# Kernel optimization log

Hardware: AMD Instinct MI355X
Metric: run time of the kernel (lower is better)

Reference implementation:

```python
import jax, jax.numpy as jnp
import numpy as np

V = 30522   # bert-base-uncased vocab
E = 512     # embed_size
ATT = 512   # attention_dim
ENC = 2048  # encoder_dim
H = 512     # decoder_dim
B = 32
N = 49      # num image features (7x7)
T = 21      # caption length -> 20 decode steps


def setup_inputs() -> dict:
    key = jax.random.key(0)
    ks = jax.random.split(key, 12)
    s = lambda i, shape: jax.random.normal(ks[i], shape, jnp.float32) * 0.02
    features = jax.random.normal(ks[0], (B, N, ENC), jnp.float32)
    captions = jax.random.randint(ks[1], (B, T), 0, V, dtype=jnp.int32)
    return dict(
        features=features, captions=captions,
        emb=s(2, (V, E)),
        W_w=s(3, (ATT, H)), W_b=jnp.zeros((ATT,), jnp.float32),
        U_w=s(4, (ATT, ENC)), U_b=jnp.zeros((ATT,), jnp.float32),
        A_w=s(5, (1, ATT)), A_b=jnp.zeros((1,), jnp.float32),
        init_h_w=s(6, (H, ENC)), init_h_b=jnp.zeros((H,), jnp.float32),
        init_c_w=s(7, (H, ENC)), init_c_b=jnp.zeros((H,), jnp.float32),
        w_ih=s(8, (4 * H, E + ENC)), w_hh=s(9, (4 * H, H)),
        b_ih=jnp.zeros((4 * H,), jnp.float32), b_hh=jnp.zeros((4 * H,), jnp.float32),
        fcn_w=s(10, (V, H)), fcn_b=jnp.zeros((V,), jnp.float32),
    )


def reference(features, captions, emb, W_w, W_b, U_w, U_b, A_w, A_b,
              init_h_w, init_h_b, init_c_w, init_c_b,
              w_ih, w_hh, b_ih, b_hh, fcn_w, fcn_b):
    embeds = emb[captions]                      # [B, T, E]
    mean_f = features.mean(axis=1)              # [B, ENC]
    h0 = mean_f @ init_h_w.T + init_h_b         # [B, H]
    c0 = mean_f @ init_c_w.T + init_c_b
    # U(features) is h-independent: precompute once (same math as per-step in torch)
    u_hs = jnp.einsum('bne,ae->bna', features, U_w) + U_b  # [B, N, ATT]

    def step(carry, x_t):
        h, c = carry
        # Bahdanau attention
        w_ah = h @ W_w.T + W_b                               # [B, ATT]
        scores = jnp.tanh(u_hs + w_ah[:, None, :]) @ A_w[0] + A_b[0]  # [B, N]
        alpha = jax.nn.softmax(scores, axis=1)
        context = jnp.einsum('bn,bne->be', alpha, features)  # [B, ENC]
        # LSTMCell (torch gate order: i, f, g, o)
        lstm_in = jnp.concatenate([x_t, context], axis=1)    # [B, E+ENC]
        gates = lstm_in @ w_ih.T + b_ih + h @ w_hh.T + b_hh  # [B, 4H]
        i, f, g, o = jnp.split(gates, 4, axis=1)
        c2 = jax.nn.sigmoid(f) * c + jax.nn.sigmoid(i) * jnp.tanh(g)
        h2 = jax.nn.sigmoid(o) * jnp.tanh(c2)
        # dropout in eval mode = identity
        out = h2 @ fcn_w.T + fcn_b                           # [B, V]
        return (h2, c2), (out, alpha)

    xs = jnp.swapaxes(embeds[:, :-1], 0, 1)  # [T-1, B, E]
    _, (preds, alphas) = jax.lax.scan(step, (h0, c0), xs)
    return jnp.swapaxes(preds, 0, 1), jnp.swapaxes(alphas, 0, 1)
```

## Files before the change

### kernel.cpp

```cpp
#include <hip/hip_runtime.h>
#include <hip/hip_bf16.h>

#define VCB 30522
#define EMB 512
#define ATTD 512
#define ENC 2048
#define HD 512
#define BB 32
#define NF 49
#define TSTEPS 20
#define EIN 2560
#define KCAT 3072
#define WSTRIDE 3080
#define DTPB 512

typedef __attribute__((ext_vector_type(8))) __bf16 bf16x8;
typedef __attribute__((ext_vector_type(4))) __bf16 bf16x4;
typedef __attribute__((ext_vector_type(4))) float floatx4;
typedef __hip_bfloat16 bf16;

__device__ __forceinline__ float bf2f(bf16 x){ return __bfloat162float(x); }
__device__ __forceinline__ bf16 f2bf(float x){ return __float2bfloat16(x); }
__device__ __forceinline__ float sigm(float x){ return 1.0f/(1.0f+expf(-x)); }
__device__ __forceinline__ float fast_tanh(float x){
    float e2 = __expf(2.0f*x);
    return 1.0f - 2.0f*__builtin_amdgcn_rcpf(e2 + 1.0f);
}

__device__ __forceinline__ float ld1(const void* base, size_t idx, int f){
    if (f) return ((const float*)base)[idx];
    return bf2f(((const bf16*)base)[idx]);
}
__device__ __forceinline__ bf16x8 ldbf8(const void* base, size_t idx, int f){
    if (f){
        const float* p = (const float*)base + idx;
        float4 a = *(const float4*)p, b = *(const float4*)(p+4);
        bf16x8 r;
        r[0]=(__bf16)a.x; r[1]=(__bf16)a.y; r[2]=(__bf16)a.z; r[3]=(__bf16)a.w;
        r[4]=(__bf16)b.x; r[5]=(__bf16)b.y; r[6]=(__bf16)b.z; r[7]=(__bf16)b.w;
        return r;
    }
    return *(const bf16x8*)((const bf16*)base + idx);
}
__device__ __forceinline__ bf16x8 bf8_of_f32(const float* p){
    float4 a = *(const float4*)p, b = *(const float4*)(p+4);
    bf16x8 r;
    r[0]=(__bf16)a.x; r[1]=(__bf16)a.y; r[2]=(__bf16)a.z; r[3]=(__bf16)a.w;
    r[4]=(__bf16)b.x; r[5]=(__bf16)b.y; r[6]=(__bf16)b.z; r[7]=(__bf16)b.w;
    return r;
}
__device__ __forceinline__ void st1(void* base, size_t idx, float v, int f){
    if (f) ((float*)base)[idx] = v;
    else   ((bf16*)base)[idx] = f2bf(v);
}

#define MFMA16(a,b,c) __builtin_amdgcn_mfma_f32_16x16x32_bf16(a,b,c,0,0,0)

__device__ __forceinline__ void gbar(unsigned* bar, unsigned ep){
    __syncthreads();
    if (threadIdx.x == 0){
        unsigned tgt = ep*16u;
        unsigned* grp  = bar + ((blockIdx.x >> 4) << 4);
        unsigned* root = bar + 256;
        unsigned old = __hip_atomic_fetch_add(grp, 1u, __ATOMIC_ACQ_REL, __HIP_MEMORY_SCOPE_AGENT);
        if (old + 1u == tgt)
            __hip_atomic_fetch_add(root, 1u, __ATOMIC_ACQ_REL, __HIP_MEMORY_SCOPE_AGENT);
        while (__hip_atomic_load(root, __ATOMIC_RELAXED, __HIP_MEMORY_SCOPE_AGENT) < tgt)
            __builtin_amdgcn_s_sleep(2);
        __builtin_amdgcn_fence(__ATOMIC_ACQUIRE, "agent");
    }
    __syncthreads();
}

__global__ void k_detect(const void* emb, int* flag, unsigned* bar){
    int tid = threadIdx.x;
    __shared__ int bad;
    if (tid == 0) bad = 0;
    for (int i = tid; i < 512; i += 256) bar[i] = 0u;
    __syncthreads();
    const unsigned short* u = (const unsigned short*)emb;
    int local = 0;
    for (int i = tid; i < 4096; i += 256){
        int e = (u[i] >> 7) & 0xFF;
        if (e > 140) local = 1;
    }
    if (local) bad = 1;
    __syncthreads();
    if (tid == 0) *flag = bad;
}

__global__ void k_prep_gates(const void* w_ih, const void* w_hh, bf16* __restrict__ wcat,
                             const int* __restrict__ flag){
    int ff = *flag;
    int r = blockIdx.x, tid = threadIdx.x;
    for (int i = tid*8; i < KCAT; i += 2048){
        bf16x8 v;
        if (i + 8 <= EIN){
            v = ldbf8(w_ih, (size_t)r*EIN + i, ff);
        } else if (i >= EIN){
            v = ldbf8(w_hh, (size_t)r*HD + (i - EIN), ff);
        } else {
#pragma unroll
            for (int j = 0; j < 8; ++j){
                int k = i + j;
                v[j] = (__bf16)((k < EIN) ? ld1(w_ih, (size_t)r*EIN + k, ff)
                                          : ld1(w_hh, (size_t)r*HD + (k - EIN), ff));
            }
        }
        *(bf16x8*)(wcat + (size_t)r*KCAT + i) = v;
    }
}
__global__ void k_prep_cvt8(const void* src, bf16* __restrict__ dst, size_t n8,
                            const int* __restrict__ flag){
    int ff = *flag;
    size_t idx = (size_t)blockIdx.x*256 + threadIdx.x;
    size_t stride = (size_t)gridDim.x*256;
    for (size_t i = idx; i < n8; i += stride)
        *(bf16x8*)(dst + i*8) = ldbf8(src, i*8, ff);
}

__global__ void k_mean(const void* feat, float* __restrict__ mean_f,
                       const int* __restrict__ flag){
    int ff = *flag;
    int b = blockIdx.x, tid = threadIdx.x;
    for (int i = 0; i < ENC/256; ++i){
        int e = i*256 + tid;
        size_t base = (size_t)b*NF*ENC + e;
        float s = 0.f;
        for (int n = 0; n < NF; ++n) s += ld1(feat, base + (size_t)n*ENC, ff);
        mean_f[b*ENC + e] = s * (1.0f/49.0f);
    }
}

__global__ void k_init_hc(const float* __restrict__ mean_f,
                          const void* ihw, const void* ihb,
                          const void* icw, const void* icb,
                          float* __restrict__ Hbuf, float* __restrict__ c_f32,
                          const int* __restrict__ flag){
    int ff = *flag;
    int tid = threadIdx.x, wave = tid>>6, lane = tid&63, quad = lane>>4, lq = lane&15;
    int n0 = blockIdx.x*16;
    int ng = n0 + lq;
    const void* w = (ng < HD) ? ihw : icw;
    size_t wrow = (size_t)(ng < HD ? ng : ng - HD)*ENC;
    floatx4 acc[2] = {{0,0,0,0},{0,0,0,0}};
    int kb = wave*512;
    for (int kk = 0; kk < 16; ++kk){
        int k = kb + kk*32 + quad*8;
        bf16x8 bfr = ldbf8(w, wrow + k, ff);
#pragma unroll
        for (int mt = 0; mt < 2; ++mt){
            bf16x8 afr = bf8_of_f32(mean_f + (size_t)(mt*16+lq)*ENC + k);
            acc[mt] = MFMA16(afr, bfr, acc[mt]);
        }
    }
    __shared__ float red[4][2][16][16];
#pragma unroll
    for (int mt = 0; mt < 2; ++mt)
        for (int r = 0; r < 4; ++r)
            red[wave][mt][quad*4+r][lq] = acc[mt][r];
    __syncthreads();
    for (int rep = 0; rep < 2; ++rep){
        int idx = rep*256 + tid;
        int mt = idx>>8, mm = (idx>>4)&15, nn = idx&15;
        float v = red[0][mt][mm][nn]+red[1][mt][mm][nn]+red[2][mt][mm][nn]+red[3][mt][mm][nn];
        int n_g = n0 + nn, b = mt*16 + mm;
        if (n_g < HD) Hbuf[b*HD + n_g]        = v + ld1(ihb, n_g, ff);
        else          c_f32[b*HD + (n_g-HD)]  = v + ld1(icb, n_g - HD, ff);
    }
}

__global__ void k_uhs(const bf16* __restrict__ feat_bf, const void* U_w, const void* U_b,
                      float* __restrict__ u_hs, const int* __restrict__ flag){
    int ff = *flag;
    int tid = threadIdx.x, wave = tid>>6, lane = tid&63, quad = lane>>4, lq = lane&15;
    int m0 = blockIdx.x*16;
    int n0 = blockIdx.y*64 + wave*16;
    size_t arow = (size_t)(m0+lq)*ENC;
    size_t brow = (size_t)(n0+lq)*ENC;
    floatx4 acc = {0,0,0,0};
    for (int kk = 0; kk < ENC/32; ++kk){
        int k = kk*32 + quad*8;
        bf16x8 afr = *(const bf16x8*)(feat_bf + arow + k);
        bf16x8 bfr = ldbf8(U_w,  brow + k, ff);
        acc = MFMA16(afr, bfr, acc);
    }
    float ub = ld1(U_b, n0+lq, ff);
    for (int r = 0; r < 4; ++r){
        int m = m0 + quad*4 + r;
        u_hs[(size_t)m*ATTD + n0 + lq] = acc[r] + ub;
    }
}

__global__ void __launch_bounds__(DTPB) k_decode(
        float* __restrict__ Hbuf, const float* __restrict__ c0_f32,
        const bf16* __restrict__ Ww_bf, const void* __restrict__ W_b,
        const float* __restrict__ u_hs, const void* __restrict__ A_w,
        const void* __restrict__ A_b, const int* __restrict__ captions,
        const void* __restrict__ emb, const bf16* __restrict__ feat_bf,
        bf16* __restrict__ lstm_in, const bf16* __restrict__ wcat,
        const void* __restrict__ b_ih, const void* __restrict__ b_hh,
        bf16* __restrict__ Hall_bf, void* __restrict__ d_out,
        const int* __restrict__ flag, unsigned* __restrict__ bar)
{
    const int ff = *flag;
    const int bid = blockIdx.x, tid = threadIdx.x;
    const int wave = tid>>6, lane = tid&63, quad = lane>>4, lq = lane&15;

    __shared__ bf16  wlds[8*WSTRIDE];
    __shared__ float ubuf[2048];
    __shared__ float aw_s[ATTD];
    __shared__ float c_loc[64];
    __shared__ float gbias[8];

    for (int n = 0; n < 8; ++n){
        int g = n>>1, j = n&1;
        const bf16* src = wcat + (size_t)(g*HD + (bid<<1) + j)*KCAT;
        for (int c8 = tid; c8 < KCAT/8; c8 += DTPB)
            *(bf16x8*)(wlds + n*WSTRIDE + c8*8) = *(const bf16x8*)(src + c8*8);
    }
    if (tid < 64){
        int bb = tid&31, j = tid>>5, col = (bid<<1)+j;
        c_loc[bb*2+j] = c0_f32[bb*HD + col];
        lstm_in[(size_t)bb*KCAT + EIN + col] = f2bf(Hbuf[bb*HD + col]);
    }
    if (tid < 8){
        int g = tid>>1, j = tid&1, col = (bid<<1)+j;
        gbias[tid] = ld1(b_ih, g*HD+col, ff) + ld1(b_hh, g*HD+col, ff);
    }
    if (bid < BB)
        for (int i = tid; i < ATTD; i += DTPB) aw_s[i] = ld1(A_w, i, ff);
    __syncthreads();

    float* h_sh    = ubuf;
    float* wah_s   = ubuf + 512;
    float* sc_s    = ubuf + 1024;
    float* alpha_s = ubuf + 1088;
    float (*red)[2][16][16] = (float (*)[2][16][16])ubuf;

    unsigned ep = 0;

    for (int t = 0; t < TSTEPS; ++t){
        if (bid < BB){
            const int b = bid;
            const float* h_t = Hbuf + (size_t)t*BB*HD;
            for (int i = tid; i < HD; i += DTPB) h_sh[i] = h_t[b*HD + i];
            int cap = captions[b*21 + t];
            for (int e = tid; e < EMB; e += DTPB)
                lstm_in[(size_t)b*KCAT + e] = f2bf(ld1(emb, (size_t)cap*EMB + e, ff));
            __syncthreads();
            for (int a = tid; a < ATTD; a += DTPB){
                const bf16* wr = Ww_bf + (size_t)a*HD;
                float s0=0.f, s1=0.f, s2=0.f, s3=0.f;
                for (int k = 0; k < HD; k += 8){
                    bf16x8 wv = *(const bf16x8*)(wr + k);
                    s0 += (float)wv[0]*h_sh[k+0] + (float)wv[4]*h_sh[k+4];
                    s1 += (float)wv[1]*h_sh[k+1] + (float)wv[5]*h_sh[k+5];
                    s2 += (float)wv[2]*h_sh[k+2] + (float)wv[6]*h_sh[k+6];
                    s3 += (float)wv[3]*h_sh[k+3] + (float)wv[7]*h_sh[k+7];
                }
                wah_s[a] = ((s0+s1)+(s2+s3)) + ld1(W_b, a, ff);
            }
            __syncthreads();
            {
                int a0 = lane*8;
                for (int n = wave; n < NF; n += 8){
                    const float* up = u_hs + (size_t)(b*NF + n)*ATTD + a0;
                    float4 u0 = *(const float4*)up;
                    float4 u1 = *(const float4*)(up + 4);
                    float p0 = fast_tanh(u0.x + wah_s[a0+0])*aw_s[a0+0]
                             + fast_tanh(u0.y + wah_s[a0+1])*aw_s[a0+1]
                             + fast_tanh(u0.z + wah_s[a0+2])*aw_s[a0+2]
                             + fast_tanh(u0.w + wah_s[a0+3])*aw_s[a0+3];
                    float p1 = fast_tanh(u1.x + wah_s[a0+4])*aw_s[a0+4]
                             + fast_tanh(u1.y + wah_s[a0+5])*aw_s[a0+5]
                             + fast_tanh(u1.z + wah_s[a0+6])*aw_s[a0+6]
                             + fast_tanh(u1.w + wah_s[a0+7])*aw_s[a0+7];
                    float p = p0 + p1;
                    for (int off = 32; off; off >>= 1) p += __shfl_down(p, off);
                    if (lane == 0) sc_s[n] = p + ld1(A_b, 0, ff);
                }
            }
            __syncthreads();
            if (wave == 0){
                float v = (lane < NF) ? sc_s[lane] : -1e30f;
                float mx = v;
                for (int off = 32; off; off >>= 1) mx = fmaxf(mx, __shfl_down(mx, off));
                mx = __shfl(mx, 0);
                float e = (lane < NF) ? expf(v - mx) : 0.f;
                float s = e;
                for (int off = 32; off; off >>= 1) s += __shfl_down(s, off);
                s = __shfl(s, 0);
                if (lane < NF){
                    float al = e / s;
                    alpha_s[lane] = al;
                    st1(d_out, (size_t)BB*TSTEPS*VCB + (size_t)b*(TSTEPS*NF) + t*NF + lane, al, ff);
                }
            }
            __syncthreads();
            {
                int e0 = tid*4;
                float acc[4] = {0,0,0,0};
#pragma unroll 7
                for (int n = 0; n < NF; ++n){
                    float al = alpha_s[n];
                    bf16x4 v = *(const bf16x4*)(feat_bf + (size_t)b*NF*ENC + (size_t)n*ENC + e0);
#pragma unroll
                    for (int j = 0; j < 4; ++j) acc[j] += al*(float)v[j];
                }
                bf16x4 st;
#pragma unroll
                for (int j = 0; j < 4; ++j) st[j] = (__bf16)acc[j];
                *(bf16x4*)(lstm_in + (size_t)b*KCAT + EMB + e0) = st;
            }
        }
        gbar(bar, ++ep);

        if (wave < 4){
            int kb = wave*768;
            floatx4 acc0 = {0,0,0,0}, acc1 = {0,0,0,0};
            const bf16* wrow = wlds + (size_t)(lq&7)*WSTRIDE;
            const bf16* ar0 = lstm_in + (size_t)lq*KCAT;
            const bf16* ar1 = lstm_in + (size_t)(16+lq)*KCAT;
#pragma unroll
            for (int kk = 0; kk < 24; ++kk){
                int k = kb + kk*32 + quad*8;
                bf16x8 bfr = *(const bf16x8*)(wrow + k);
                acc0 = MFMA16(*(const bf16x8*)(ar0 + k), bfr, acc0);
                acc1 = MFMA16(*(const bf16x8*)(ar1 + k), bfr, acc1);
            }
#pragma unroll
            for (int r = 0; r < 4; ++r){
                red[wave][0][quad*4+r][lq] = acc0[r];
                red[wave][1][quad*4+r][lq] = acc1[r];
            }
        }
        __syncthreads();
        if (tid < 64){
            int bb = tid&31, j = tid>>5;
            int mt = bb>>4, mm = bb&15;
            float G[4];
#pragma unroll
            for (int g = 0; g < 4; ++g){
                int n = g*2 + j;
                G[g] = red[0][mt][mm][n] + red[1][mt][mm][n]
                     + red[2][mt][mm][n] + red[3][mt][mm][n] + gbias[n];
            }
            float c_old = c_loc[bb*2+j];
            float c_new = sigm(G[1])*c_old + sigm(G[0])*tanhf(G[2]);
            float h_new = sigm(G[3])*tanhf(c_new);
            c_loc[bb*2+j] = c_new;
            int col = (bid<<1)+j;
            Hbuf[(size_t)(t+1)*BB*HD + bb*HD + col] = h_new;
            Hall_bf[(size_t)t*BB*HD + bb*HD + col]  = f2bf(h_new);
            lstm_in[(size_t)bb*KCAT + EIN + col]    = f2bf(h_new);
        }
        gbar(bar, ++ep);
    }
}

__global__ void __launch_bounds__(256) k_fcn(const bf16* __restrict__ Hall_bf,
                                             const bf16* __restrict__ fcnw_bf,
                                             const void* fcn_b, void* d_out,
                                             const int* __restrict__ flag){
    int ff = *flag;
    int tid = threadIdx.x, wave = tid>>6, lane = tid&63, quad = lane>>4, lq = lane&15;
    int n0 = blockIdx.x*64 + wave*16;
    int v = n0 + lq;
    int vc = (v < VCB) ? v : (VCB-1);
    const bf16* brow = fcnw_bf + (size_t)vc*HD;
    bf16x8 bfr[16];
#pragma unroll
    for (int kk = 0; kk < 16; ++kk) bfr[kk] = *(const bf16x8*)(brow + kk*32 + quad*8);
    float bias = ld1(fcn_b, vc, ff);
    for (int mt = 0; mt < 40; ++mt){
        const bf16* arow = Hall_bf + (size_t)(mt*16 + lq)*HD;
        floatx4 acc = {0,0,0,0};
#pragma unroll
        for (int kk = 0; kk < 16; ++kk){
            bf16x8 afr = *(const bf16x8*)(arow + kk*32 + quad*8);
            acc = MFMA16(afr, bfr[kk], acc);
        }
        if (v < VCB){
#pragma unroll
            for (int r = 0; r < 4; ++r){
                int m = mt*16 + quad*4 + r;
                int b = m & 31, tt = m >> 5;
                st1(d_out, (size_t)b*(TSTEPS*VCB) + (size_t)tt*VCB + v, acc[r] + bias, ff);
            }
        }
    }
}

extern "C" void kernel_launch(void* const* d_in, const int* in_sizes, int n_in,
                              void* d_out, int out_size, void* d_ws, size_t ws_size,
                              hipStream_t stream) {
    const void* feat  = d_in[0];
    const int*  caps  = (const int*)d_in[1];
    const void* emb   = d_in[2];
    const void* W_w   = d_in[3];
    const void* W_b   = d_in[4];
    const void* U_w   = d_in[5];
    const void* U_b   = d_in[6];
    const void* A_w   = d_in[7];
    const void* A_b   = d_in[8];
    const void* ihw   = d_in[9];
    const void* ihb   = d_in[10];
    const void* icw   = d_in[11];
    const void* icb   = d_in[12];
    const void* w_ih  = d_in[13];
    const void* w_hh  = d_in[14];
    const void* b_ih  = d_in[15];
    const void* b_hh  = d_in[16];
    const void* fcn_w = d_in[17];
    const void* fcn_b = d_in[18];

    char* ws = (char*)d_ws;
    size_t off = 0;
    float* u_hs    = (float*)(ws + off); off += (size_t)BB*NF*ATTD*4;
    float* c_f32   = (float*)(ws + off); off += (size_t)BB*HD*4;
    float* mean_f  = (float*)(ws + off); off += (size_t)BB*ENC*4;
    float* Hbuf    = (float*)(ws + off); off += (size_t)(TSTEPS+1)*BB*HD*4;
    bf16*  lstm_in = (bf16*) (ws + off); off += (size_t)BB*KCAT*2;
    bf16*  Hall_bf = (bf16*) (ws + off); off += (size_t)TSTEPS*BB*HD*2;
    bf16*  wcat    = (bf16*) (ws + off); off += (size_t)4*HD*KCAT*2;
    bf16*  fcnw_bf = (bf16*) (ws + off); off += (size_t)VCB*HD*2;
    bf16*  Ww_bf   = (bf16*) (ws + off); off += (size_t)ATTD*HD*2;
    bf16*  feat_bf = (bf16*) (ws + off); off += (size_t)BB*NF*ENC*2;
    int*   flag    = (int*)  (ws + off); off += 256;
    unsigned* bar  = (unsigned*)(ws + off); off += 2048;
    if (ws_size < off) return;

    k_detect    <<<1, 256, 0, stream>>>(emb, flag, bar);
    k_prep_gates<<<2048, 256, 0, stream>>>(w_ih, w_hh, wcat, flag);
    k_prep_cvt8 <<<2048, 256, 0, stream>>>(fcn_w, fcnw_bf, (size_t)VCB*HD/8, flag);
    k_prep_cvt8 <<<128, 256, 0, stream>>>(W_w, Ww_bf, (size_t)ATTD*HD/8, flag);
    k_prep_cvt8 <<<1024, 256, 0, stream>>>(feat, feat_bf, (size_t)BB*NF*ENC/8, flag);
    k_mean      <<<BB, 256, 0, stream>>>(feat, mean_f, flag);
    k_init_hc   <<<64, 256, 0, stream>>>(mean_f, ihw, ihb, icw, icb, Hbuf, c_f32, flag);
    k_uhs       <<<dim3(98, 8), 256, 0, stream>>>(feat_bf, U_w, U_b, u_hs, flag);

    {
        void* kargs[18] = {
            (void*)&Hbuf, (void*)&c_f32, (void*)&Ww_bf, (void*)&W_b,
            (void*)&u_hs, (void*)&A_w, (void*)&A_b, (void*)&caps,
            (void*)&emb, (void*)&feat_bf, (void*)&lstm_in, (void*)&wcat,
            (void*)&b_ih, (void*)&b_hh, (void*)&Hall_bf, (void*)&d_out,
            (void*)&flag, (void*)&bar
        };
        hipLaunchCooperativeKernel((void*)k_decode, dim3(256), dim3(DTPB),
                                   kargs, 0, stream);
    }

    k_fcn<<<477, 256, 0, stream>>>(Hall_bf, fcnw_bf, fcn_b, d_out, flag);
}
```

Before: 1.649 ms.

## Halve decode grid to 128 blocks, use coherent atomics instead of barrier fences

The cooperative decode kernel now runs on 128 blocks, each owning four hidden columns (16 gate rows held in LDS) instead of two. This halves the number of blocks taking part in each grid barrier, and all 16 MFMA B-columns now carry useful gate rows. Shared activations (lstm_in, Hbuf) are read and written through relaxed agent-scope atomic loads and stores, so the barrier drops its acq_rel ordering and acquire fence. In exchange, each block does twice the gate work, and the scalar 32-bit coherent loads replace vector loads in the MFMA loop. Correctness now depends on relaxed atomics giving enough ordering.

```diff
diff --git a/kernel.cpp b/kernel.cpp
--- a/kernel.cpp
+++ b/kernel.cpp
@@ -13,6 +13,8 @@
 #define KCAT 3072
 #define WSTRIDE 3080
 #define DTPB 512
+#define NBLK 128
+#define NGRP 8
 
 typedef __attribute__((ext_vector_type(8))) __bf16 bf16x8;
 typedef __attribute__((ext_vector_type(4))) __bf16 bf16x4;
@@ -25,6 +27,18 @@
 __device__ __forceinline__ float fast_tanh(float x){
     float e2 = __expf(2.0f*x);
     return 1.0f - 2.0f*__builtin_amdgcn_rcpf(e2 + 1.0f);
+}
+
+__device__ __forceinline__ unsigned coh_ld(const unsigned* p){
+    return __hip_atomic_load(p, __ATOMIC_RELAXED, __HIP_MEMORY_SCOPE_AGENT);
+}
+__device__ __forceinline__ void coh_st(unsigned* p, unsigned v){
+    __hip_atomic_store(p, v, __ATOMIC_RELAXED, __HIP_MEMORY_SCOPE_AGENT);
+}
+__device__ __forceinline__ unsigned pack2bf(float a, float b){
+    unsigned short ua = __builtin_bit_cast(unsigned short, f2bf(a));
+    unsigned short ub = __builtin_bit_cast(unsigned short, f2bf(b));
+    return (unsigned)ua | ((unsigned)ub << 16);
 }
 
 __device__ __forceinline__ float ld1(const void* base, size_t idx, int f){
@@ -59,15 +73,13 @@
 __device__ __forceinline__ void gbar(unsigned* bar, unsigned ep){
     __syncthreads();
     if (threadIdx.x == 0){
-        unsigned tgt = ep*16u;
         unsigned* grp  = bar + ((blockIdx.x >> 4) << 4);
         unsigned* root = bar + 256;
-        unsigned old = __hip_atomic_fetch_add(grp, 1u, __ATOMIC_ACQ_REL, __HIP_MEMORY_SCOPE_AGENT);
-        if (old + 1u == tgt)
-            __hip_atomic_fetch_add(root, 1u, __ATOMIC_ACQ_REL, __HIP_MEMORY_SCOPE_AGENT);
-        while (__hip_atomic_load(root, __ATOMIC_RELAXED, __HIP_MEMORY_SCOPE_AGENT) < tgt)
+        unsigned old = __hip_atomic_fetch_add(grp, 1u, __ATOMIC_RELAXED, __HIP_MEMORY_SCOPE_AGENT);
+        if (old + 1u == ep*16u)
+            __hip_atomic_fetch_add(root, 1u, __ATOMIC_RELAXED, __HIP_MEMORY_SCOPE_AGENT);
+        while (__hip_atomic_load(root, __ATOMIC_RELAXED, __HIP_MEMORY_SCOPE_AGENT) < ep*NGRP)
             __builtin_amdgcn_s_sleep(2);
-        __builtin_amdgcn_fence(__ATOMIC_ACQUIRE, "agent");
     }
     __syncthreads();
 }
@@ -207,25 +219,32 @@
     const int bid = blockIdx.x, tid = threadIdx.x;
     const int wave = tid>>6, lane = tid&63, quad = lane>>4, lq = lane&15;
 
-    __shared__ bf16  wlds[8*WSTRIDE];
+    __shared__ bf16  wlds[16*WSTRIDE];
     __shared__ float ubuf[2048];
     __shared__ float aw_s[ATTD];
-    __shared__ float c_loc[64];
-    __shared__ float gbias[8];
-
-    for (int n = 0; n < 8; ++n){
-        int g = n>>1, j = n&1;
-        const bf16* src = wcat + (size_t)(g*HD + (bid<<1) + j)*KCAT;
+    __shared__ float c_loc[BB*4];
+    __shared__ float gbias[16];
+
+    unsigned* lin_u = (unsigned*)lstm_in;
+
+    for (int n = 0; n < 16; ++n){
+        int g = n>>2, j = n&3;
+        const bf16* src = wcat + (size_t)(g*HD + (bid<<2) + j)*KCAT;
         for (int c8 = tid; c8 < KCAT/8; c8 += DTPB)
             *(bf16x8*)(wlds + n*WSTRIDE + c8*8) = *(const bf16x8*)(src + c8*8);
     }
+    if (tid < 128){
+        int bb = tid&31, j = tid>>5, col = (bid<<2)+j;
+        c_loc[bb*4+j] = c0_f32[bb*HD + col];
+    }
     if (tid < 64){
-        int bb = tid&31, j = tid>>5, col = (bid<<1)+j;
-        c_loc[bb*2+j] = c0_f32[bb*HD + col];
-        lstm_in[(size_t)bb*KCAT + EIN + col] = f2bf(Hbuf[bb*HD + col]);
-    }
-    if (tid < 8){
-        int g = tid>>1, j = tid&1, col = (bid<<1)+j;
+        int bb = tid&31, j2 = tid>>5;
+        int c0 = (bid<<2) + 2*j2;
+        float h0 = Hbuf[bb*HD + c0], h1 = Hbuf[bb*HD + c0 + 1];
+        coh_st(lin_u + (size_t)bb*(KCAT/2) + (EIN + c0)/2, pack2bf(h0, h1));
+    }
+    if (tid < 16){
+        int g = tid>>2, j = tid&3, col = (bid<<2)+j;
         gbias[tid] = ld1(b_ih, g*HD+col, ff) + ld1(b_hh, g*HD+col, ff);
     }
     if (bid < BB)
@@ -243,11 +262,15 @@
     for (int t = 0; t < TSTEPS; ++t){
         if (bid < BB){
             const int b = bid;
-            const float* h_t = Hbuf + (size_t)t*BB*HD;
-            for (int i = tid; i < HD; i += DTPB) h_sh[i] = h_t[b*HD + i];
+            const unsigned* hrow = (const unsigned*)(Hbuf + (size_t)t*BB*HD + b*HD);
+            for (int i = tid; i < HD; i += DTPB)
+                h_sh[i] = __uint_as_float(coh_ld(hrow + i));
             int cap = captions[b*21 + t];
-            for (int e = tid; e < EMB; e += DTPB)
-                lstm_in[(size_t)b*KCAT + e] = f2bf(ld1(emb, (size_t)cap*EMB + e, ff));
+            for (int e2 = tid; e2 < EMB/2; e2 += DTPB){
+                float a = ld1(emb, (size_t)cap*EMB + 2*e2,     ff);
+                float c = ld1(emb, (size_t)cap*EMB + 2*e2 + 1, ff);
+                coh_st(lin_u + (size_t)b*(KCAT/2) + e2, pack2bf(a, c));
+            }
             __syncthreads();
             for (int a = tid; a < ATTD; a += DTPB){
                 const bf16* wr = Ww_bf + (size_t)a*HD;
@@ -308,10 +331,9 @@
 #pragma unroll
                     for (int j = 0; j < 4; ++j) acc[j] += al*(float)v[j];
                 }
-                bf16x4 st;
-#pragma unroll
-                for (int j = 0; j < 4; ++j) st[j] = (__bf16)acc[j];
-                *(bf16x4*)(lstm_in + (size_t)b*KCAT + EMB + e0) = st;
+                unsigned* lrow = lin_u + (size_t)b*(KCAT/2) + (EMB + e0)/2;
+                coh_st(lrow,     pack2bf(acc[0], acc[1]));
+                coh_st(lrow + 1, pack2bf(acc[2], acc[3]));
             }
         }
         gbar(bar, ++ep);
@@ -319,15 +341,22 @@
         if (wave < 4){
             int kb = wave*768;
             floatx4 acc0 = {0,0,0,0}, acc1 = {0,0,0,0};
-            const bf16* wrow = wlds + (size_t)(lq&7)*WSTRIDE;
-            const bf16* ar0 = lstm_in + (size_t)lq*KCAT;
-            const bf16* ar1 = lstm_in + (size_t)(16+lq)*KCAT;
+            const bf16* wrow = wlds + (size_t)lq*WSTRIDE;
+            const unsigned* ar0 = lin_u + (size_t)lq*(KCAT/2);
+            const unsigned* ar1 = lin_u + (size_t)(16+lq)*(KCAT/2);
+            union U8 { unsigned u[4]; bf16x8 v; };
 #pragma unroll
             for (int kk = 0; kk < 24; ++kk){
-                int k = kb + kk*32 + quad*8;
-                bf16x8 bfr = *(const bf16x8*)(wrow + k);
-                acc0 = MFMA16(*(const bf16x8*)(ar0 + k), bfr, acc0);
-                acc1 = MFMA16(*(const bf16x8*)(ar1 + k), bfr, acc1);
+                int kd = (kb + kk*32 + quad*8) >> 1;
+                bf16x8 bfr = *(const bf16x8*)(wrow + kb + kk*32 + quad*8);
+                U8 a0, a1;
+#pragma unroll
+                for (int q = 0; q < 4; ++q){
+                    a0.u[q] = coh_ld(ar0 + kd + q);
+                    a1.u[q] = coh_ld(ar1 + kd + q);
+                }
+                acc0 = MFMA16(a0.v, bfr, acc0);
+                acc1 = MFMA16(a1.v, bfr, acc1);
             }
 #pragma unroll
             for (int r = 0; r < 4; ++r){
@@ -337,23 +366,31 @@
         }
         __syncthreads();
         if (tid < 64){
-            int bb = tid&31, j = tid>>5;
+            int bb = tid&31, j2 = tid>>5;
             int mt = bb>>4, mm = bb&15;
-            float G[4];
-#pragma unroll
-            for (int g = 0; g < 4; ++g){
-                int n = g*2 + j;
-                G[g] = red[0][mt][mm][n] + red[1][mt][mm][n]
-                     + red[2][mt][mm][n] + red[3][mt][mm][n] + gbias[n];
-            }
-            float c_old = c_loc[bb*2+j];
-            float c_new = sigm(G[1])*c_old + sigm(G[0])*tanhf(G[2]);
-            float h_new = sigm(G[3])*tanhf(c_new);
-            c_loc[bb*2+j] = c_new;
-            int col = (bid<<1)+j;
-            Hbuf[(size_t)(t+1)*BB*HD + bb*HD + col] = h_new;
-            Hall_bf[(size_t)t*BB*HD + bb*HD + col]  = f2bf(h_new);
-            lstm_in[(size_t)bb*KCAT + EIN + col]    = f2bf(h_new);
+            float hn[2];
+#pragma unroll
+            for (int sub = 0; sub < 2; ++sub){
+                int j = 2*j2 + sub;
+                float G[4];
+#pragma unroll
+                for (int g = 0; g < 4; ++g){
+                    int n = g*4 + j;
+                    G[g] = red[0][mt][mm][n] + red[1][mt][mm][n]
+                         + red[2][mt][mm][n] + red[3][mt][mm][n] + gbias[n];
+                }
+                float c_old = c_loc[bb*4+j];
+                float c_new = sigm(G[1])*c_old + sigm(G[0])*tanhf(G[2]);
+                float h_new = sigm(G[3])*tanhf(c_new);
+                c_loc[bb*4+j] = c_new;
+                hn[sub] = h_new;
+            }
+            int colb = (bid<<2) + 2*j2;
+            unsigned* hb = (unsigned*)(Hbuf + (size_t)(t+1)*BB*HD + bb*HD + colb);
+            coh_st(hb,     __float_as_uint(hn[0]));
+            coh_st(hb + 1, __float_as_uint(hn[1]));
+            ((unsigned*)Hall_bf)[((size_t)t*BB*HD + bb*HD + colb) >> 1] = pack2bf(hn[0], hn[1]);
+            coh_st(lin_u + (size_t)bb*(KCAT/2) + (EIN + colb)/2, pack2bf(hn[0], hn[1]));
         }
         gbar(bar, ++ep);
     }
@@ -448,7 +485,7 @@
             (void*)&b_ih, (void*)&b_hh, (void*)&Hall_bf, (void*)&d_out,
             (void*)&flag, (void*)&bar
         };
-        hipLaunchCooperativeKernel((void*)k_decode, dim3(256), dim3(DTPB),
+        hipLaunchCooperativeKernel((void*)k_decode, dim3(NBLK), dim3(DTPB),
                                    kargs, 0, stream);
     }
 
```

Measured after the change: 1.550 ms. 1.06x faster.
